# Kernel tuning notes

Hardware: AMD Instinct MI355X
Metric: run time of the kernel (lower is better)

Reference implementation:

```python
import jax, jax.numpy as jnp
import numpy as np

K = 3  # kernel_size


def conv2d_same(x, w, b):
    # x: NHWC, w: HWIO
    y = jax.lax.conv_general_dilated(
        x, w, window_strides=(1, 1), padding='SAME',
        dimension_numbers=('NHWC', 'HWIO', 'NHWC'))
    return y + b


def setup_inputs() -> dict:
    key = jax.random.key(0)
    k0, k1, k2 = jax.random.split(key, 3)
    B, H, Wd, C, F = 8, 128, 128, 64, 128
    x = jax.random.normal(k0, (B, H, Wd, C), jnp.float32)
    # offset conv: small random weights (zeros in original init -> degenerate),
    # scaled down so offsets stay in a realistic few-pixel range
    W_off = jax.random.normal(k1, (K, K, C, 2 * K * K), jnp.float32) * 0.01
    b_off = jnp.zeros((2 * K * K,), jnp.float32)
    fan_in = K * K * K * K * C
    W = jax.random.normal(k2, (K, K, K * K * C, F), jnp.float32) / np.float32(np.sqrt(fan_in))
    b = jnp.zeros((F,), jnp.float32)
    return {"x": x, "W_off": W_off, "b_off": b_off, "W": W, "b": b}


def reference(x, W_off, b_off, W, b):
    B, H, Wd, C = x.shape
    KK = K * K
    # predicted per-pixel, per-tap (dx, dy) offsets
    offsets = conv2d_same(x, W_off, b_off).reshape(B, H, Wd, KK, 2)

    # base pixel grid, stacked as (x, y) like the original
    gy, gx = jnp.meshgrid(jnp.arange(H, dtype=jnp.float32),
                          jnp.arange(Wd, dtype=jnp.float32), indexing='ij')
    grid = jnp.stack([gx, gy], axis=-1)[None, :, :, None, :]  # (1,H,W,1,2)

    # kernel tap grid, 'xy' meshgrid like tf.meshgrid default
    off = (K - 1) / 2.0
    lin = jnp.linspace(-off, off, K).astype(jnp.float32)
    kx, ky = jnp.meshgrid(lin, lin)
    kgrid = jnp.stack([kx, ky], axis=-1).reshape(1, 1, 1, KK, 2)

    loc = grid + kgrid + offsets  # (B,H,W,KK,2)
    lx = jnp.clip(loc[..., 0], 0.0, Wd - 1.0)
    ly = jnp.clip(loc[..., 1], 0.0, H - 1.0)

    x0 = jnp.clip(jnp.floor(lx), 0.0, Wd - 1.0)
    x1 = jnp.clip(jnp.floor(lx) + 1.0, 0.0, Wd - 1.0)
    y0 = jnp.clip(jnp.floor(ly), 0.0, H - 1.0)
    y1 = jnp.clip(jnp.floor(ly) + 1.0, 0.0, H - 1.0)

    # weights computed from the CLIPPED corner coords, as in the original
    wa = (x1 - lx) * (y1 - ly)
    wb = (x1 - lx) * (ly - y0)
    wc = (lx - x0) * (y1 - ly)
    wd = (lx - x0) * (ly - y0)

    x0i, x1i = x0.astype(jnp.int32), x1.astype(jnp.int32)
    y0i, y1i = y0.astype(jnp.int32), y1.astype(jnp.int32)

    xf = x.reshape(B, H * Wd, C)

    def gather(yi, xi):
        idx = (yi * Wd + xi).reshape(B, -1)           # (B, H*W*KK)
        g = jax.vmap(lambda f, i: f[i])(xf, idx)      # (B, P, C)
        return g.reshape(B, H, Wd, KK, C)

    Ia = gather(y0i, x0i)
    Ib = gather(y1i, x0i)
    Ic = gather(y0i, x1i)
    Id = gather(y1i, x1i)

    sampled = (wa[..., None] * Ia + wb[..., None] * Ib
               + wc[..., None] * Ic + wd[..., None] * Id)
    sampled = sampled.reshape(B, H, Wd, KK * C)
    return conv2d_same(sampled, W, b)
```

## Files before the change

kernel.cpp:

```cpp
#include <hip/hip_runtime.h>
#include <hip/hip_bf16.h>

#define B_   8
#define H_   128
#define W_   128
#define C_   64
#define F_   128
#define KDIM 5184
#define BHW_ 131072

#define TH   8
#define TW   16
#define HY   10
#define HX   18
#define NPX  180

#define STILE 0
#define BTILE 11520
#define PARMW 36096
#define PARMO 37536
#define LDSSZ 38976

typedef __bf16 bf16x8 __attribute__((ext_vector_type(8)));
typedef float  f32x4  __attribute__((ext_vector_type(4)));

__device__ __forceinline__ unsigned short f2bf(float f) {
  unsigned int u = __float_as_uint(f);
  unsigned int r = (u + 0x7fffu + ((u >> 16) & 1u)) >> 16;
  return (unsigned short)r;
}

__global__ __launch_bounds__(256) void woff_prep_kernel(
    const float* __restrict__ Woff, unsigned short* __restrict__ WbHi,
    unsigned short* __restrict__ WbLo) {
  int u = blockIdx.x * 256 + threadIdx.x;
  if (u >= 18432) return;
  int j  = u & 7;
  int kq = (u >> 3) & 3;
  int n  = (u >> 5) & 15;
  int nt = (u >> 9) & 1;
  int tc = u >> 10;
  int tap = tc >> 1, kch = tc & 1;
  int o = nt * 16 + n;
  int c = kch * 32 + kq * 8 + j;
  float val = 0.f;
  if (o < 18) val = Woff[(tap * 64 + c) * 18 + o];
  unsigned short h = f2bf(val);
  float hf = __uint_as_float((unsigned)h << 16);
  WbHi[u] = h;
  WbLo[u] = f2bf(val - hf);
}

__global__ __launch_bounds__(256, 3) void offs_mfma_kernel(
    const float* __restrict__ x, const unsigned short* __restrict__ WbHi,
    const unsigned short* __restrict__ WbLo, const float* __restrict__ boff,
    float* __restrict__ offsP) {
  __shared__ __align__(16) short lds[26112];
  const int tid = threadIdx.x, lane = tid & 63, w = tid >> 6;
  const int bid = blockIdx.x;
  const int b  = bid >> 7;
  const int t  = bid & 127;
  const int r4 = t >> 2, cq = t & 3;
  const int gy0 = r4 * 4, gx0 = cq * 32;
  const float* xb = x + (size_t)b * (H_ * W_ * C_);

#pragma unroll
  for (int it = 0; it < 7; ++it) {
    int u = it * 256 + tid;
    if (u < 1632) {
      int p = u >> 3, j = u & 7;
      int rowi = p / 34, coli = p - rowi * 34;
      int gy = gy0 - 1 + rowi, gx = gx0 - 1 + coli;
      union { unsigned short s[8]; uint4 v; } hi, lo;
      if ((unsigned)gy < (unsigned)H_ && (unsigned)gx < (unsigned)W_) {
        const float* src = xb + (((gy << 7) + gx) << 6) + j * 8;
        float4 v0 = ((const float4*)src)[0], v1 = ((const float4*)src)[1];
        float f[8] = {v0.x, v0.y, v0.z, v0.w, v1.x, v1.y, v1.z, v1.w};
#pragma unroll
        for (int e = 0; e < 8; ++e) {
          unsigned short h16 = f2bf(f[e]);
          hi.s[e] = h16;
          lo.s[e] = f2bf(f[e] - __uint_as_float((unsigned)h16 << 16));
        }
      } else {
        hi.v = make_uint4(0, 0, 0, 0);
        lo.v = hi.v;
      }
      int a = p * 64 + ((j ^ (coli & 7)) * 8);
      *(uint4*)&lds[a] = hi.v;
      *(uint4*)&lds[13056 + a] = lo.v;
    }
  }
  __syncthreads();

  const int l15 = lane & 15, kq = lane >> 4;
  const int bbase = (l15 * 4 + kq) * 8;
  f32x4 acc[2][2] = {};

#pragma unroll
  for (int ky = 0; ky < 3; ++ky) {
#pragma unroll
    for (int kx = 0; kx < 3; ++kx) {
      const int tap = ky * 3 + kx;
#pragma unroll
      for (int kch = 0; kch < 2; ++kch) {
        const int tc = tap * 2 + kch;
        bf16x8 bh0 = *(const bf16x8*)&WbHi[tc * 1024 + bbase];
        bf16x8 bh1 = *(const bf16x8*)&WbHi[tc * 1024 + 512 + bbase];
        bf16x8 bl0 = *(const bf16x8*)&WbLo[tc * 1024 + bbase];
        bf16x8 bl1 = *(const bf16x8*)&WbLo[tc * 1024 + 512 + bbase];
#pragma unroll
        for (int mt = 0; mt < 2; ++mt) {
          int coli = mt * 16 + l15 + kx;
          int px = (w + ky) * 34 + coli;
          int a = px * 64 + (((kch * 4 + kq) ^ (coli & 7)) * 8);
          bf16x8 ah = *(const bf16x8*)&lds[a];
          bf16x8 al = *(const bf16x8*)&lds[13056 + a];
          acc[mt][0] = __builtin_amdgcn_mfma_f32_16x16x32_bf16(ah, bh0, acc[mt][0], 0, 0, 0);
          acc[mt][0] = __builtin_amdgcn_mfma_f32_16x16x32_bf16(al, bh0, acc[mt][0], 0, 0, 0);
          acc[mt][0] = __builtin_amdgcn_mfma_f32_16x16x32_bf16(ah, bl0, acc[mt][0], 0, 0, 0);
          acc[mt][1] = __builtin_amdgcn_mfma_f32_16x16x32_bf16(ah, bh1, acc[mt][1], 0, 0, 0);
          acc[mt][1] = __builtin_amdgcn_mfma_f32_16x16x32_bf16(al, bh1, acc[mt][1], 0, 0, 0);
          acc[mt][1] = __builtin_amdgcn_mfma_f32_16x16x32_bf16(ah, bl1, acc[mt][1], 0, 0, 0);
        }
      }
    }
  }

  __syncthreads();
  float* accbuf = (float*)lds;
  float bv0 = boff[l15];
  float bv1 = boff[min(16 + l15, 17)];
#pragma unroll
  for (int mt = 0; mt < 2; ++mt)
#pragma unroll
    for (int r = 0; r < 4; ++r) {
      int px = mt * 16 + kq * 4 + r;
      accbuf[(w * 32 + px) * 19 + l15] = acc[mt][0][r] + bv0;
      if (l15 < 2)
        accbuf[(w * 32 + px) * 19 + 16 + l15] = acc[mt][1][r] + bv1;
    }
  __syncthreads();
  const int lane32 = tid & 31, tpi = tid >> 5;
#pragma unroll
  for (int v = 0; v < 9; ++v) {
    int u = v * 8 + tpi;
    int o = u >> 2, w2 = u & 3;
    float val = accbuf[(w2 * 32 + lane32) * 19 + o];
    offsP[(size_t)o * BHW_ + (size_t)b * 16384 + (gy0 + w2) * 128 + gx0 + lane32] = val;
  }
}

__global__ __launch_bounds__(256) void wt_prep_kernel(
    const float* __restrict__ Wf, unsigned short* __restrict__ Wt) {
  __shared__ float Wl[64][65];
  const int tid = threadIdx.x;
  const int kk0 = (blockIdx.x % 81) * 64;
  const int f0  = (blockIdx.x / 81) * 64;
  for (int i = tid; i < 4096; i += 256) {
    int kk = i >> 6, f = i & 63;
    Wl[kk][f] = Wf[(size_t)(kk0 + kk) * F_ + f0 + f];
  }
  __syncthreads();
  for (int i = tid; i < 4096; i += 256) {
    int f = i >> 6, kk = i & 63;
    Wt[(size_t)(f0 + f) * KDIM + kk0 + kk] = f2bf(Wl[kk][f]);
  }
}

__global__ __launch_bounds__(256, 2) void fused_kernel(
    const float* __restrict__ x, const float* __restrict__ offsP,
    const unsigned short* __restrict__ Wt, const float* __restrict__ bias,
    float* __restrict__ out) {
  __shared__ __align__(16) short lds[LDSSZ];
  const int tid  = threadIdx.x;
  const int lane = tid & 63;
  const int wv   = tid >> 6;
  const int gr   = (blockIdx.x & 7) * 128 + (blockIdx.x >> 3);
  const int b    = gr >> 7;
  const int tile = gr & 127;
  const int ty   = tile >> 3, tx = tile & 7;
  const int gy0  = ty * TH, gx0 = tx * TW;
  const float* xb = x + (size_t)b * (H_ * W_ * C_);

  const int l15  = lane & 15, quad = lane >> 4;
  const int sub  = lane & 7,  rig  = lane >> 3;
  const int wm   = (wv >> 1) * 64, wn = (wv & 1) * 64;

  f32x4 acc[4][4] = {};

  int p0[4];
#pragma unroll
  for (int i = 0; i < 4; ++i) p0[i] = ((wv >> 1) * 4 + i) * HX + l15;
  int bo[2][4];
#pragma unroll
  for (int ks = 0; ks < 2; ++ks)
#pragma unroll
    for (int j = 0; j < 4; ++j)
      bo[ks][j] = BTILE + (wn + 16 * j + l15) * 64 + (((ks * 4 + quad) ^ (l15 & 7)) * 8);

  const int s_py = tid / HX, s_px = tid - s_py * HX;

  for (int t = 0; t < 9; ++t) {
    __syncthreads();
    if (tid < NPX) {
      int gy = gy0 + s_py - 1, gx = gx0 + s_px - 1;
      float wa = 0.f, wb = 0.f, wc = 0.f, wd = 0.f;
      int oA = 0, oB = 0, oC = 0, oD = 0;
      if ((unsigned)gy < (unsigned)H_ && (unsigned)gx < (unsigned)W_) {
        int pix = (b * H_ + gy) * W_ + gx;
        float offx = offsP[(size_t)(2 * t) * BHW_ + pix];
        float offy = offsP[(size_t)(2 * t + 1) * BHW_ + pix];
        float lx = (float)gx + (float)(t % 3 - 1) + offx;
        float ly = (float)gy + (float)(t / 3 - 1) + offy;
        lx = fminf(fmaxf(lx, 0.f), 127.f);
        ly = fminf(fmaxf(ly, 0.f), 127.f);
        float fx = floorf(lx), fy = floorf(ly);
        float x0c = fminf(fmaxf(fx, 0.f), 127.f);
        float x1c = fminf(fmaxf(fx + 1.f, 0.f), 127.f);
        float y0c = fminf(fmaxf(fy, 0.f), 127.f);
        float y1c = fminf(fmaxf(fy + 1.f, 0.f), 127.f);
        wa = (x1c - lx) * (y1c - ly);
        wb = (x1c - lx) * (ly - y0c);
        wc = (lx - x0c) * (y1c - ly);
        wd = (lx - x0c) * (ly - y0c);
        int ix0 = (int)x0c, ix1 = (int)x1c, iy0 = (int)y0c, iy1 = (int)y1c;
        oA = (iy0 * W_ + ix0) * C_;
        oB = (iy1 * W_ + ix0) * C_;
        oC = (iy0 * W_ + ix1) * C_;
        oD = (iy1 * W_ + ix1) * C_;
      }
      ((float4*)&lds[PARMW])[tid] = make_float4(wa, wb, wc, wd);
      ((int4*)&lds[PARMO])[tid]  = make_int4(oA | (s_px << 20), oB, oC, oD);
    }
    __syncthreads();
#pragma unroll
    for (int it = 0; it < 6; ++it) {
      int u = it * 256 + tid;
      if (u < NPX * 8) {
        int p = u >> 3, j = u & 7;
        float4 wv4 = ((const float4*)&lds[PARMW])[p];
        int4   ov4 = ((const int4*)&lds[PARMO])[p];
        int pxl = ov4.x >> 20;
        const float* pa = xb + (ov4.x & 0xFFFFF) + j * 8;
        const float* pb = xb + ov4.y + j * 8;
        const float* pc = xb + ov4.z + j * 8;
        const float* pd = xb + ov4.w + j * 8;
        float4 A0 = ((const float4*)pa)[0], A1 = ((const float4*)pa)[1];
        float4 B0 = ((const float4*)pb)[0], B1 = ((const float4*)pb)[1];
        float4 C0 = ((const float4*)pc)[0], C1 = ((const float4*)pc)[1];
        float4 D0 = ((const float4*)pd)[0], D1 = ((const float4*)pd)[1];
        union { unsigned short s[8]; uint4 v; } uu;
        uu.s[0] = f2bf(wv4.x * A0.x + wv4.y * B0.x + wv4.z * C0.x + wv4.w * D0.x);
        uu.s[1] = f2bf(wv4.x * A0.y + wv4.y * B0.y + wv4.z * C0.y + wv4.w * D0.y);
        uu.s[2] = f2bf(wv4.x * A0.z + wv4.y * B0.z + wv4.z * C0.z + wv4.w * D0.z);
        uu.s[3] = f2bf(wv4.x * A0.w + wv4.y * B0.w + wv4.z * C0.w + wv4.w * D0.w);
        uu.s[4] = f2bf(wv4.x * A1.x + wv4.y * B1.x + wv4.z * C1.x + wv4.w * D1.x);
        uu.s[5] = f2bf(wv4.x * A1.y + wv4.y * B1.y + wv4.z * C1.y + wv4.w * D1.y);
        uu.s[6] = f2bf(wv4.x * A1.z + wv4.y * B1.z + wv4.z * C1.z + wv4.w * D1.z);
        uu.s[7] = f2bf(wv4.x * A1.w + wv4.y * B1.w + wv4.z * C1.w + wv4.w * D1.w);
        *(uint4*)&lds[STILE + p * 64 + ((j ^ (pxl & 7)) * 8)] = uu.v;
      }
    }
    for (int g = 0; g < 3; ++g) {
      __syncthreads();
#pragma unroll
      for (int i = 0; i < 12; ++i) {
        int slot = wv * 12 + i;
        int chunk = slot >> 4;
        int f = ((slot & 15) * 8) + rig;
        int tap2 = g * 3 + chunk;
        const short* src = (const short*)Wt + (size_t)f * KDIM +
                           tap2 * 576 + t * 64 + ((sub ^ rig) * 8);
        __builtin_amdgcn_global_load_lds(
            (const __attribute__((address_space(1))) void*)src,
            (__attribute__((address_space(3))) void*)&lds[BTILE + slot * 512],
            16, 0, 0);
      }
      __syncthreads();
      const int off2 = g * HX;
#pragma unroll
      for (int c3 = 0; c3 < 3; ++c3) {
        int t1 = (l15 + c3) & 7;
        int xr0 = ((quad ^ t1) * 8);
        int xr1 = (((4 + quad) ^ t1) * 8);
#pragma unroll
        for (int ks = 0; ks < 2; ++ks) {
          int xr = ks ? xr1 : xr0;
          bf16x8 af[4], bfr[4];
#pragma unroll
          for (int i = 0; i < 4; ++i)
            af[i] = *(const bf16x8*)&lds[(p0[i] + off2 + c3) * 64 + xr];
#pragma unroll
          for (int j = 0; j < 4; ++j)
            bfr[j] = *(const bf16x8*)&lds[bo[ks][j] + c3 * 8192];
#pragma unroll
          for (int i = 0; i < 4; ++i)
#pragma unroll
            for (int j = 0; j < 4; ++j)
              acc[i][j] = __builtin_amdgcn_mfma_f32_16x16x32_bf16(
                  af[i], bfr[j], acc[i][j], 0, 0, 0);
        }
      }
    }
  }

  float bj[4];
#pragma unroll
  for (int j = 0; j < 4; ++j) bj[j] = bias[wn + 16 * j + l15];
#pragma unroll
  for (int i = 0; i < 4; ++i) {
    int gy = gy0 + (wv >> 1) * 4 + i;
#pragma unroll
    for (int r = 0; r < 4; ++r) {
      int gx = gx0 + quad * 4 + r;
      float* rp = out + ((size_t)((b * H_ + gy) * W_ + gx)) * F_;
#pragma unroll
      for (int j = 0; j < 4; ++j)
        rp[wn + 16 * j + l15] = acc[i][j][r] + bj[j];
    }
  }
}

extern "C" void kernel_launch(void* const* d_in, const int* in_sizes, int n_in,
                              void* d_out, int out_size, void* d_ws, size_t ws_size,
                              hipStream_t stream) {
  (void)in_sizes; (void)n_in; (void)out_size; (void)ws_size;
  const float* x    = (const float*)d_in[0];
  const float* Woff = (const float*)d_in[1];
  const float* boff = (const float*)d_in[2];
  const float* Wf   = (const float*)d_in[3];
  const float* bias = (const float*)d_in[4];
  float* out = (float*)d_out;

  char* ws = (char*)d_ws;
  size_t off_bytes = (size_t)18 * BHW_ * 4;
  size_t p1 = (off_bytes + 255) & ~(size_t)255;
  size_t wt_bytes = (size_t)F_ * KDIM * 2;
  float*          offsP = (float*)ws;
  unsigned short* Wt    = (unsigned short*)(ws + p1);
  unsigned short* WbHi  = (unsigned short*)(ws + p1 + wt_bytes);
  unsigned short* WbLo  = WbHi + 18432;

  woff_prep_kernel<<<72, 256, 0, stream>>>(Woff, WbHi, WbLo);
  offs_mfma_kernel<<<1024, 256, 0, stream>>>(x, WbHi, WbLo, boff, offsP);
  wt_prep_kernel<<<162, 256, 0, stream>>>(Wf, Wt);
  fused_kernel<<<1024, 256, 0, stream>>>(x, offsP, Wt, bias, out);
}
```

Baseline: 306.5 us.

## Double-buffer weight tiles per tap and cache A fragments in registers

```diff
diff --git a/kernel.cpp b/kernel.cpp
--- a/kernel.cpp
+++ b/kernel.cpp
@@ -16,10 +16,11 @@
 #define NPX  180
 
 #define STILE 0
-#define BTILE 11520
-#define PARMW 36096
-#define PARMO 37536
-#define LDSSZ 38976
+#define BT0   11520
+#define BT1   19712
+#define PARMW 27904
+#define PARMO 29344
+#define LDSSZ 30784
 
 typedef __bf16 bf16x8 __attribute__((ext_vector_type(8)));
 typedef float  f32x4  __attribute__((ext_vector_type(4)));
@@ -185,24 +186,32 @@
 
   const int l15  = lane & 15, quad = lane >> 4;
   const int sub  = lane & 7,  rig  = lane >> 3;
-  const int wm   = (wv >> 1) * 64, wn = (wv & 1) * 64;
+  const int wn   = (wv & 1) * 64;
+  const int mbase = (wv >> 1) * 4;
 
   f32x4 acc[4][4] = {};
 
-  int p0[4];
-#pragma unroll
-  for (int i = 0; i < 4; ++i) p0[i] = ((wv >> 1) * 4 + i) * HX + l15;
   int bo[2][4];
 #pragma unroll
   for (int ks = 0; ks < 2; ++ks)
 #pragma unroll
     for (int j = 0; j < 4; ++j)
-      bo[ks][j] = BTILE + (wn + 16 * j + l15) * 64 + (((ks * 4 + quad) ^ (l15 & 7)) * 8);
+      bo[ks][j] = (wn + 16 * j + l15) * 64 + (((ks * 4 + quad) ^ (l15 & 7)) * 8);
 
   const int s_py = tid / HX, s_px = tid - s_py * HX;
 
+#pragma unroll
+  for (int i = 0; i < 4; ++i) {
+    int slot = wv * 4 + i;
+    int f = slot * 8 + rig;
+    const short* src = (const short*)Wt + (size_t)f * KDIM + ((sub ^ rig) * 8);
+    __builtin_amdgcn_global_load_lds(
+        (const __attribute__((address_space(1))) void*)src,
+        (__attribute__((address_space(3))) void*)&lds[BT0 + slot * 512],
+        16, 0, 0);
+  }
+
   for (int t = 0; t < 9; ++t) {
-    __syncthreads();
     if (tid < NPX) {
       int gy = gy0 + s_py - 1, gx = gx0 + s_px - 1;
       float wa = 0.f, wb = 0.f, wc = 0.f, wd = 0.f;
@@ -262,46 +271,60 @@
         *(uint4*)&lds[STILE + p * 64 + ((j ^ (pxl & 7)) * 8)] = uu.v;
       }
     }
-    for (int g = 0; g < 3; ++g) {
-      __syncthreads();
-#pragma unroll
-      for (int i = 0; i < 12; ++i) {
-        int slot = wv * 12 + i;
-        int chunk = slot >> 4;
-        int f = ((slot & 15) * 8) + rig;
-        int tap2 = g * 3 + chunk;
-        const short* src = (const short*)Wt + (size_t)f * KDIM +
-                           tap2 * 576 + t * 64 + ((sub ^ rig) * 8);
-        __builtin_amdgcn_global_load_lds(
-            (const __attribute__((address_space(1))) void*)src,
-            (__attribute__((address_space(3))) void*)&lds[BTILE + slot * 512],
-            16, 0, 0);
-      }
-      __syncthreads();
-      const int off2 = g * HX;
-#pragma unroll
-      for (int c3 = 0; c3 < 3; ++c3) {
-        int t1 = (l15 + c3) & 7;
-        int xr0 = ((quad ^ t1) * 8);
-        int xr1 = (((4 + quad) ^ t1) * 8);
+    __syncthreads();
+
+    bf16x8 areg[3][2][6];
+#pragma unroll
+    for (int c3 = 0; c3 < 3; ++c3) {
+      const int t1 = (l15 + c3) & 7;
+#pragma unroll
+      for (int ks = 0; ks < 2; ++ks) {
+        const int xr = ((ks * 4 + quad) ^ t1) * 8;
+#pragma unroll
+        for (int rr = 0; rr < 6; ++rr)
+          areg[c3][ks][rr] =
+              *(const bf16x8*)&lds[((mbase + rr) * HX + l15 + c3) * 64 + xr];
+      }
+    }
+
+#pragma unroll
+    for (int cc = 0; cc < 9; ++cc) {
+      const int cur = ((t + cc) & 1) ? BT1 : BT0;
+      if (t < 8 || cc < 8) {
+        const int nxt = ((t + cc) & 1) ? BT0 : BT1;
+        const int ngc = (cc + 1) % 9;
+        const int ntt = t + (cc == 8 ? 1 : 0);
+#pragma unroll
+        for (int i = 0; i < 4; ++i) {
+          int slot = wv * 4 + i;
+          int f = slot * 8 + rig;
+          const short* src = (const short*)Wt + (size_t)f * KDIM +
+                             ngc * 576 + ntt * 64 + ((sub ^ rig) * 8);
+          __builtin_amdgcn_global_load_lds(
+              (const __attribute__((address_space(1))) void*)src,
+              (__attribute__((address_space(3))) void*)&lds[nxt + slot * 512],
+              16, 0, 0);
+        }
+      }
+      {
+        const int g = cc / 3, c3m = cc % 3;
+        __builtin_amdgcn_s_setprio(1);
 #pragma unroll
         for (int ks = 0; ks < 2; ++ks) {
-          int xr = ks ? xr1 : xr0;
-          bf16x8 af[4], bfr[4];
-#pragma unroll
-          for (int i = 0; i < 4; ++i)
-            af[i] = *(const bf16x8*)&lds[(p0[i] + off2 + c3) * 64 + xr];
+          bf16x8 bfr[4];
 #pragma unroll
           for (int j = 0; j < 4; ++j)
-            bfr[j] = *(const bf16x8*)&lds[bo[ks][j] + c3 * 8192];
+            bfr[j] = *(const bf16x8*)&lds[cur + bo[ks][j]];
 #pragma unroll
           for (int i = 0; i < 4; ++i)
 #pragma unroll
             for (int j = 0; j < 4; ++j)
               acc[i][j] = __builtin_amdgcn_mfma_f32_16x16x32_bf16(
-                  af[i], bfr[j], acc[i][j], 0, 0, 0);
+                  areg[c3m][ks][i + g], bfr[j], acc[i][j], 0, 0, 0);
         }
-      }
+        __builtin_amdgcn_s_setprio(0);
+      }
+      __syncthreads();
     }
   }
 
@@ -310,7 +333,7 @@
   for (int j = 0; j < 4; ++j) bj[j] = bias[wn + 16 * j + l15];
 #pragma unroll
   for (int i = 0; i < 4; ++i) {
-    int gy = gy0 + (wv >> 1) * 4 + i;
+    int gy = gy0 + mbase + i;
 #pragma unroll
     for (int r = 0; r < 4; ++r) {
       int gx = gx0 + quad * 4 + r;
```

Measured after the change: 393.0 us. +28.2%, slower.
